# Kernel tuning notes

Measured on AMD Instinct MI355X. Metric: run time of the kernel, lower is better.

Reference implementation:

```python
import jax, jax.numpy as jnp
import numpy as np

B = 65536      # batch
IN = 784       # 1*28*28 flattened input
H = 768        # hidden_size
D = 3          # num_domains
E = 64         # expert hidden
C = 10         # classes
EPS = 1e-5     # BatchNorm eps


def setup_inputs() -> dict:
    key = jax.random.key(0)
    ks = jax.random.split(key, 8)
    s = lambda k, shp, sc: (jax.random.normal(k, shp, jnp.float32) * sc)
    return dict(
        x=jax.random.normal(ks[0], (B, 1, 28, 28), jnp.float32),
        # pre_classifier: Linear(784, H) + BatchNorm1d(H) affine params
        W1=s(ks[1], (IN, H), 0.03), b1=jnp.zeros((H,), jnp.float32),
        gamma=jnp.ones((H,), jnp.float32), beta=jnp.zeros((H,), jnp.float32),
        # discriminator: Linear(H,H) -> ReLU -> Linear(H,D)
        Wd1=s(ks[2], (H, H), 0.03), bd1=jnp.zeros((H,), jnp.float32),
        Wd2=s(ks[3], (H, D), 0.03), bd2=jnp.zeros((D,), jnp.float32),
        # per-domain expert classifiers: Linear(H,64) -> ReLU -> Linear(64,10), stacked over D
        Wa=s(ks[4], (D, H, E), 0.03), ba=jnp.zeros((D, E), jnp.float32),
        Wb=s(ks[5], (D, E, C), 0.1), bb=jnp.zeros((D, C), jnp.float32),
    )


def reference(x, W1, b1, gamma, beta, Wd1, bd1, Wd2, bd2, Wa, ba, Wb, bb):
    xf = x.reshape(x.shape[0], -1)                      # [B, 784]
    h = xf @ W1 + b1                                    # [B, H]
    # BatchNorm1d in training mode: batch mean / biased variance
    mu = h.mean(axis=0)
    var = jnp.mean((h - mu) ** 2, axis=0)
    feat = jax.nn.relu((h - mu) / jnp.sqrt(var + EPS) * gamma + beta)  # [B, H]
    # ReverseLayerF with alpha=0: identity forward, zero gradient back to feat
    rev = jax.lax.stop_gradient(feat)
    dom_out = jax.nn.relu(rev @ Wd1 + bd1) @ Wd2 + bd2  # [B, D]
    dom_pred = jnp.argmax(dom_out, axis=1)              # [B] int routing
    # hard routing: compute all D tiny experts densely, select by dom_pred
    hid = jax.nn.relu(jnp.einsum('bh,dhe->bde', feat, Wa) + ba)   # [B, D, E]
    all_out = jnp.einsum('bde,dec->bdc', hid, Wb) + bb            # [B, D, C]
    outs = jnp.take_along_axis(all_out, dom_pred[:, None, None], axis=1)[:, 0, :]  # [B, C]
    return outs, dom_out
```

## Files before the change

### kernel.cpp

```cpp
#include <hip/hip_runtime.h>
#include <math.h>

#define BATCH 65536
#define KIN   784
#define HD    768

typedef float f32x4 __attribute__((ext_vector_type(4)));
typedef short s16x8 __attribute__((ext_vector_type(8)));
typedef unsigned int __attribute__((address_space(3))) lds_u32;
typedef const unsigned int __attribute__((address_space(1))) glb_u32;

__device__ __forceinline__ float frelu(float x){ return x > 0.f ? x : 0.f; }

__device__ __forceinline__ unsigned int cvtpk(float a, float b){
    unsigned int r;
    asm("v_cvt_pk_bf16_f32 %0, %1, %2" : "=v"(r) : "v"(a), "v"(b));
    return r;
}
__device__ __forceinline__ unsigned short f2bf(float v){
    unsigned int u = __builtin_bit_cast(unsigned int, v);
    u += 0x7FFFu + ((u >> 16) & 1u);
    return (unsigned short)(u >> 16);
}
__device__ __forceinline__ float bf2f(unsigned short s){
    unsigned int u = ((unsigned int)s) << 16;
    return __builtin_bit_cast(float, u);
}
__device__ __forceinline__ void gload16(const void* g, void* l){
    __builtin_amdgcn_global_load_lds((glb_u32*)g, (lds_u32*)l, 16, 0, 0);
}

__global__ __launch_bounds__(256)
void cvtX(const float* __restrict__ x, unsigned short* __restrict__ xbf)
{
    int idx = blockIdx.x * 256 + threadIdx.x;
    int row = idx / 104, c = (idx - row * 104) * 8;
    uint4 o = make_uint4(0, 0, 0, 0);
    if (c < KIN) {
        const float* p = x + (size_t)row * KIN + c;
        float4 a = *(const float4*)p;
        float4 b = *(const float4*)(p + 4);
        o.x = cvtpk(a.x, a.y); o.y = cvtpk(a.z, a.w);
        o.z = cvtpk(b.x, b.y); o.w = cvtpk(b.z, b.w);
    }
    *(uint4*)(xbf + (size_t)row * 832 + c) = o;
}

__global__ __launch_bounds__(256)
void featBN(const unsigned short* __restrict__ hbf,
            const float* __restrict__ scale, const float* __restrict__ shift,
            unsigned short* __restrict__ fbf)
{
    int idx = blockIdx.x * 256 + threadIdx.x;
    int row = idx / 96, c = (idx - row * 96) * 8;
    s16x8 hv = *(const s16x8*)(hbf + (size_t)row * HD + c);
    float4 s0 = *(const float4*)(scale + c), s1 = *(const float4*)(scale + c + 4);
    float4 t0 = *(const float4*)(shift + c), t1 = *(const float4*)(shift + c + 4);
    float v[8];
    v[0] = frelu(bf2f((unsigned short)hv[0]) * s0.x + t0.x);
    v[1] = frelu(bf2f((unsigned short)hv[1]) * s0.y + t0.y);
    v[2] = frelu(bf2f((unsigned short)hv[2]) * s0.z + t0.z);
    v[3] = frelu(bf2f((unsigned short)hv[3]) * s0.w + t0.w);
    v[4] = frelu(bf2f((unsigned short)hv[4]) * s1.x + t1.x);
    v[5] = frelu(bf2f((unsigned short)hv[5]) * s1.y + t1.y);
    v[6] = frelu(bf2f((unsigned short)hv[6]) * s1.z + t1.z);
    v[7] = frelu(bf2f((unsigned short)hv[7]) * s1.w + t1.w);
    uint4 o;
    o.x = cvtpk(v[0], v[1]); o.y = cvtpk(v[2], v[3]);
    o.z = cvtpk(v[4], v[5]); o.w = cvtpk(v[6], v[7]);
    *(uint4*)(fbf + (size_t)row * HD + c) = o;
}

__global__ __launch_bounds__(256)
void tileW(const float* __restrict__ W, char* __restrict__ Wh, int K, int N, int NT)
{
    int chunk = blockIdx.x;
    int nb = chunk / NT, t = chunk - nb * NT;
    int tid = threadIdx.x;
    #pragma unroll
    for (int q = 0; q < 2; q++) {
        int idx = q * 256 + tid;
        int r = idx >> 2, p = idx & 3;
        int s = (p ^ ((r >> 1) & 3)) & 3;
        int kb = t * 32 + s * 8;
        int n = nb * 128 + r;
        s16x8 hv;
        #pragma unroll
        for (int e = 0; e < 8; e++) {
            int k = kb + e;
            float v = (k < K) ? W[(size_t)k * N + n] : 0.f;
            hv[e] = (short)f2bf(v);
        }
        *(s16x8*)(Wh + (size_t)chunk * 8192 + idx * 16) = hv;
    }
}

__global__ __launch_bounds__(256)
void tileWa(const float* __restrict__ Wa, char* __restrict__ WaC)
{
    int chunk = blockIdx.x;
    int d = chunk / 24, t = chunk - d * 24;
    int idx = threadIdx.x;
    int r = idx >> 2, p = idx & 3;
    int s = (p ^ ((r >> 1) & 3)) & 3;
    int kb = t * 32 + s * 8;
    s16x8 hv;
    #pragma unroll
    for (int e = 0; e < 8; e++)
        hv[e] = (short)f2bf(Wa[((size_t)d * HD + kb + e) * 64 + r]);
    *(s16x8*)(WaC + (size_t)chunk * 4096 + idx * 16) = hv;
}

template<int MODE>
__global__ __launch_bounds__(256, 3)
void gemm97(const unsigned short* __restrict__ Abf,
            const char* __restrict__ BhC,
            const float* __restrict__ bias,
            unsigned short* __restrict__ Hbf,
            const float* __restrict__ Wd2, double* __restrict__ domacc,
            float* __restrict__ sp1, float* __restrict__ sp2,
            int KP, int NT)
{
    __shared__ __align__(16) char sm[32768];

    int bid = blockIdx.x;
    int wg = (bid & 7) * 384 + (bid >> 3);
    int mb = wg / 6, nb = wg - mb * 6;
    int m0 = mb << 7, n0 = nb << 7;

    int tid = threadIdx.x;
    int lane = tid & 63, wid = tid >> 6;
    int wr = wid >> 1, wc = wid & 1;
    int l15 = lane & 15, l4 = lane >> 4;

    int aoff[4], boff[4];
    #pragma unroll
    for (int f = 0; f < 4; f++) {
        int ra = wr * 64 + f * 16 + l15;
        aoff[f] = ra * 64 + (((l4 ^ (ra >> 1)) & 3) << 4);
        int rb = wc * 64 + f * 16 + l15;
        boff[f] = rb * 64 + (((l4 ^ (rb >> 1)) & 3) << 4);
    }

    int ar[2], asl[2];
    #pragma unroll
    for (int q = 0; q < 2; q++) {
        int idx = q * 256 + tid;
        int r = idx >> 2, p = idx & 3;
        asl[q] = (p ^ ((r >> 1) & 3)) & 3;
        ar[q] = r;
    }

    f32x4 acc[4][4];
    #pragma unroll
    for (int i = 0; i < 4; i++)
        #pragma unroll
        for (int j = 0; j < 4; j++) acc[i][j] = (f32x4){0.f, 0.f, 0.f, 0.f};

    int NTc = 2 * NT;
    for (int t = 0; t < NT; t++) {
        int t2 = 2 * t;
        #pragma unroll
        for (int h = 0; h < 2; h++) {
            #pragma unroll
            for (int q = 0; q < 2; q++) {
                const unsigned short* src = Abf + (size_t)(m0 + ar[q]) * KP
                                          + (t2 + h) * 32 + asl[q] * 8;
                gload16(src, sm + h * 8192 + (q * 256 + tid) * 16);
            }
        }
        #pragma unroll
        for (int h = 0; h < 2; h++) {
            size_t cb = (size_t)(nb * NTc + t2 + h) * 8192;
            #pragma unroll
            for (int q = 0; q < 2; q++) {
                int off = (q * 256 + tid) * 16;
                gload16(BhC + cb + off, sm + 16384 + h * 8192 + off);
            }
        }
        __syncthreads();
        #pragma unroll
        for (int h = 0; h < 2; h++) {
            const char* ab  = sm + h * 8192;
            const char* bb2 = sm + 16384 + h * 8192;
            s16x8 fah[4], fbh[4];
            #pragma unroll
            for (int f = 0; f < 4; f++) {
                fah[f] = *(const s16x8*)(ab + aoff[f]);
                fbh[f] = *(const s16x8*)(bb2 + boff[f]);
            }
            #pragma unroll
            for (int i = 0; i < 4; i++)
                #pragma unroll
                for (int j = 0; j < 4; j++)
                    acc[i][j] = __builtin_amdgcn_mfma_f32_16x16x32_bf16(fah[i], fbh[j], acc[i][j], 0, 0, 0);
        }
        __syncthreads();
    }

    if (MODE == 0) {
        float bc[4];
        #pragma unroll
        for (int f = 0; f < 4; f++) bc[f] = bias[n0 + wc * 64 + f * 16 + l15];
        float cs[4] = {0.f,0.f,0.f,0.f}, cq[4] = {0.f,0.f,0.f,0.f};
        #pragma unroll
        for (int i = 0; i < 4; i++) {
            int rowb = m0 + wr * 64 + i * 16 + l4 * 4;
            #pragma unroll
            for (int j2 = 0; j2 < 4; j2++) {
                unsigned short* hrow = Hbf + (size_t)(rowb + j2) * HD + n0 + wc * 64 + l15;
                #pragma unroll
                for (int f = 0; f < 4; f++) {
                    float v = acc[i][f][j2] + bc[f];
                    hrow[f * 16] = (unsigned short)cvtpk(v, v);
                    cs[f] += v; cq[f] += v * v;
                }
            }
        }
        #pragma unroll
        for (int m = 16; m < 64; m <<= 1)
            #pragma unroll
            for (int f = 0; f < 4; f++) {
                cs[f] += __shfl_xor(cs[f], m, 64);
                cq[f] += __shfl_xor(cq[f], m, 64);
            }
        if (l4 == 0) {
            #pragma unroll
            for (int f = 0; f < 4; f++) {
                int col = n0 + wc * 64 + f * 16 + l15;
                sp1[(size_t)col * 1024 + mb * 2 + wr] = cs[f];
                sp2[(size_t)col * 1024 + mb * 2 + wr] = cq[f];
            }
        }
    } else {
        float bc[4], w2[4][3];
        #pragma unroll
        for (int f = 0; f < 4; f++) {
            int col = n0 + wc * 64 + f * 16 + l15;
            bc[f] = bias[col];
            w2[f][0] = Wd2[col * 3 + 0]; w2[f][1] = Wd2[col * 3 + 1]; w2[f][2] = Wd2[col * 3 + 2];
        }
        float s0[16], s1[16], s2[16];
        #pragma unroll
        for (int i = 0; i < 16; i++) { s0[i] = 0.f; s1[i] = 0.f; s2[i] = 0.f; }
        #pragma unroll
        for (int i = 0; i < 4; i++)
            #pragma unroll
            for (int j2 = 0; j2 < 4; j2++) {
                int idx = i * 4 + j2;
                #pragma unroll
                for (int f = 0; f < 4; f++) {
                    float v = frelu(acc[i][f][j2] + bc[f]);
                    s0[idx] += v * w2[f][0];
                    s1[idx] += v * w2[f][1];
                    s2[idx] += v * w2[f][2];
                }
            }
        #pragma unroll
        for (int m = 1; m < 16; m <<= 1) {
            #pragma unroll
            for (int i = 0; i < 16; i++) {
                s0[i] += __shfl_xor(s0[i], m, 64);
                s1[i] += __shfl_xor(s1[i], m, 64);
                s2[i] += __shfl_xor(s2[i], m, 64);
            }
        }
        if (l15 == 0) {
            #pragma unroll
            for (int i = 0; i < 16; i++) {
                int row = m0 + wr * 64 + (i >> 2) * 16 + l4 * 4 + (i & 3);
                atomicAdd(&domacc[(size_t)row * 3 + 0], (double)s0[i]);
                atomicAdd(&domacc[(size_t)row * 3 + 1], (double)s1[i]);
                atomicAdd(&domacc[(size_t)row * 3 + 2], (double)s2[i]);
            }
        }
    }
}

__global__ __launch_bounds__(256)
void bnfinal(const float* __restrict__ sp1, const float* __restrict__ sp2,
             const float* __restrict__ gamma, const float* __restrict__ beta,
             float* __restrict__ scale, float* __restrict__ shift)
{
    int c = blockIdx.x, t = threadIdx.x;
    const float* p1 = sp1 + (size_t)c * 1024;
    const float* p2 = sp2 + (size_t)c * 1024;
    double S = (double)p1[t] + (double)p1[t + 256] + (double)p1[t + 512] + (double)p1[t + 768];
    double Q = (double)p2[t] + (double)p2[t + 256] + (double)p2[t + 512] + (double)p2[t + 768];
    #pragma unroll
    for (int m = 1; m < 64; m <<= 1) { S += __shfl_xor(S, m, 64); Q += __shfl_xor(Q, m, 64); }
    __shared__ double sd1[4], sd2[4];
    int w = t >> 6;
    if ((t & 63) == 0) { sd1[w] = S; sd2[w] = Q; }
    __syncthreads();
    if (t == 0) {
        double Sa = sd1[0] + sd1[1] + sd1[2] + sd1[3];
        double Qa = sd2[0] + sd2[1] + sd2[2] + sd2[3];
        double mu  = Sa * (1.0 / 65536.0);
        double var = Qa * (1.0 / 65536.0) - mu * mu;
        double inv = 1.0 / sqrt(var + 1e-5);
        double sc  = inv * (double)gamma[c];
        double sh  = (double)beta[c] - mu * sc;
        scale[c] = (float)sc;
        shift[c] = (float)sh;
    }
}

__global__ __launch_bounds__(256)
void domfinal_a(const double* __restrict__ domacc, const float* __restrict__ bd2,
                float* __restrict__ outdom, int* __restrict__ fixmeta, int* __restrict__ fixlist)
{
    int r = blockIdx.x * 256 + threadIdx.x;
    double v0 = domacc[(size_t)r * 3 + 0] + (double)bd2[0];
    double v1 = domacc[(size_t)r * 3 + 1] + (double)bd2[1];
    double v2 = domacc[(size_t)r * 3 + 2] + (double)bd2[2];
    outdom[(size_t)r * 3 + 0] = (float)v0;
    outdom[(size_t)r * 3 + 1] = (float)v1;
    outdom[(size_t)r * 3 + 2] = (float)v2;
    double mx01 = v0 > v1 ? v0 : v1, mn01 = v0 > v1 ? v1 : v0;
    double best = mx01 > v2 ? mx01 : v2;
    double m2   = mx01 > v2 ? (mn01 > v2 ? mn01 : v2) : mx01;
    if (best - m2 < 1.5e-2) {
        int p = atomicAdd(fixmeta, 1);
        fixlist[p] = r;
    }
}

#define FR 8
__global__ __launch_bounds__(256)
void fixrow_x(const int* __restrict__ fixmeta, const int* __restrict__ fixlist,
              const float* __restrict__ x, const float* __restrict__ W1,
              const float* __restrict__ b1,
              const float* __restrict__ scale, const float* __restrict__ shift,
              const float* __restrict__ Wd1, const float* __restrict__ bd1,
              const float* __restrict__ Wd2, const float* __restrict__ bd2,
              float* __restrict__ outdom)
{
    int nfix = fixmeta[0];
    __shared__ float xs[FR][788];
    __shared__ float ft[FR][HD];
    __shared__ float red[4][3];
    int tid = threadIdx.x;
    int n0 = tid * 3;
    for (int base = blockIdx.x * FR; base < nfix; base += gridDim.x * FR) {
        int nr = nfix - base; if (nr > FR) nr = FR;
        __syncthreads();
        for (int i = tid; i < FR * KIN; i += 256) {
            int rr = i / KIN, c = i - rr * KIN;
            int row = fixlist[base + (rr < nr ? rr : nr - 1)];
            xs[rr][c] = x[(size_t)row * KIN + c];
        }
        __syncthreads();
        {
            float acc[FR][3];
            #pragma unroll
            for (int r = 0; r < FR; r++) { acc[r][0]=0.f; acc[r][1]=0.f; acc[r][2]=0.f; }
            for (int k = 0; k < KIN; k++) {
                float w0 = W1[(size_t)k * HD + n0];
                float w1 = W1[(size_t)k * HD + n0 + 1];
                float w2 = W1[(size_t)k * HD + n0 + 2];
                #pragma unroll
                for (int r = 0; r < FR; r++) {
                    float xv = xs[r][k];
                    acc[r][0] += xv * w0; acc[r][1] += xv * w1; acc[r][2] += xv * w2;
                }
            }
            #pragma unroll
            for (int j = 0; j < 3; j++) {
                float bj = b1[n0 + j], scj = scale[n0 + j], shj = shift[n0 + j];
                #pragma unroll
                for (int r = 0; r < FR; r++)
                    ft[r][n0 + j] = frelu((acc[r][j] + bj) * scj + shj);
            }
        }
        __syncthreads();
        float acc[FR][3];
        #pragma unroll
        for (int r = 0; r < FR; r++) { acc[r][0]=0.f; acc[r][1]=0.f; acc[r][2]=0.f; }
        for (int k = 0; k < HD; k++) {
            float w0 = Wd1[(size_t)k * HD + n0];
            float w1 = Wd1[(size_t)k * HD + n0 + 1];
            float w2 = Wd1[(size_t)k * HD + n0 + 2];
            #pragma unroll
            for (int r = 0; r < FR; r++) {
                float fv = ft[r][k];
                acc[r][0] += fv * w0; acc[r][1] += fv * w1; acc[r][2] += fv * w2;
            }
        }
        float b0 = bd1[n0], b1v = bd1[n0 + 1], b2 = bd1[n0 + 2];
        float wa[3][3];
        #pragma unroll
        for (int i = 0; i < 3; i++)
            #pragma unroll
            for (int d = 0; d < 3; d++) wa[i][d] = Wd2[(n0 + i) * 3 + d];
        #pragma unroll
        for (int r = 0; r < FR; r++) {
            if (r >= nr) break;
            float h0 = frelu(acc[r][0] + b0);
            float h1 = frelu(acc[r][1] + b1v);
            float h2 = frelu(acc[r][2] + b2);
            float y0 = h0 * wa[0][0] + h1 * wa[1][0] + h2 * wa[2][0];
            float y1 = h0 * wa[0][1] + h1 * wa[1][1] + h2 * wa[2][1];
            float y2 = h0 * wa[0][2] + h1 * wa[1][2] + h2 * wa[2][2];
            #pragma unroll
            for (int m = 1; m < 64; m <<= 1) {
                y0 += __shfl_xor(y0, m, 64);
                y1 += __shfl_xor(y1, m, 64);
                y2 += __shfl_xor(y2, m, 64);
            }
            if ((tid & 63) == 0) { red[tid >> 6][0] = y0; red[tid >> 6][1] = y1; red[tid >> 6][2] = y2; }
            __syncthreads();
            if (tid == 0) {
                int row = fixlist[base + r];
                double v0 = (double)red[0][0] + red[1][0] + red[2][0] + red[3][0] + (double)bd2[0];
                double v1 = (double)red[0][1] + red[1][1] + red[2][1] + red[3][1] + (double)bd2[1];
                double v2 = (double)red[0][2] + red[1][2] + red[2][2] + red[3][2] + (double)bd2[2];
                outdom[(size_t)row * 3 + 0] = (float)v0;
                outdom[(size_t)row * 3 + 1] = (float)v1;
                outdom[(size_t)row * 3 + 2] = (float)v2;
            }
            __syncthreads();
        }
    }
}

__global__ __launch_bounds__(256)
void domfinal_b(const float* __restrict__ outdom, int* __restrict__ cnt, int* __restrict__ lists)
{
    __shared__ int lcnt[3], base[3];
    int tid = threadIdx.x;
    if (tid < 3) lcnt[tid] = 0;
    __syncthreads();
    int r = blockIdx.x * 256 + tid;
    float v0 = outdom[(size_t)r * 3 + 0];
    float v1 = outdom[(size_t)r * 3 + 1];
    float v2 = outdom[(size_t)r * 3 + 2];
    int p = 0; float best = v0;
    if (v1 > best) { best = v1; p = 1; }
    if (v2 > best) { best = v2; p = 2; }
    int lpos = atomicAdd(&lcnt[p], 1);
    __syncthreads();
    if (tid < 3) base[tid] = atomicAdd(&cnt[tid], lcnt[tid]);
    __syncthreads();
    lists[(size_t)p * BATCH + base[p] + lpos] = r;
}

__global__ __launch_bounds__(256)
void expert_mfma(const unsigned short* __restrict__ fbf,
                 const char* __restrict__ WaC,
                 const int* __restrict__ cnt, const int* __restrict__ lists,
                 const float* __restrict__ ba,
                 const float* __restrict__ Wb, const float* __restrict__ bb,
                 float* __restrict__ outs)
{
    __shared__ __align__(16) char sm[12288];
    __shared__ float hid[128][66];
    __shared__ int rowidx[128];

    int d = blockIdx.y;
    int count = cnt[d];
    int start = blockIdx.x * 128;
    if (start >= count) return;
    int nrows = count - start; if (nrows > 128) nrows = 128;

    int tid = threadIdx.x;
    int lane = tid & 63, wid = tid >> 6;
    int l15 = lane & 15, l4 = lane >> 4;

    if (tid < 128) {
        int i = tid < nrows ? tid : nrows - 1;
        rowidx[tid] = lists[(size_t)d * BATCH + start + i];
    }
    __syncthreads();

    int asl[2], arow[2];
    #pragma unroll
    for (int q = 0; q < 2; q++) {
        int idx = q * 256 + tid;
        int r = idx >> 2, p = idx & 3;
        asl[q] = (p ^ ((r >> 1) & 3)) & 3;
        arow[q] = rowidx[r];
    }

    int aoff[2], boff[4];
    #pragma unroll
    for (int i2 = 0; i2 < 2; i2++) {
        int ra = wid * 32 + i2 * 16 + l15;
        aoff[i2] = ra * 64 + (((l4 ^ (ra >> 1)) & 3) << 4);
    }
    #pragma unroll
    for (int f = 0; f < 4; f++) {
        int rb = f * 16 + l15;
        boff[f] = rb * 64 + (((l4 ^ (rb >> 1)) & 3) << 4);
    }

    f32x4 acc[2][4];
    #pragma unroll
    for (int i = 0; i < 2; i++)
        #pragma unroll
        for (int j = 0; j < 4; j++) acc[i][j] = (f32x4){0.f, 0.f, 0.f, 0.f};

    for (int t = 0; t < 24; t++) {
        #pragma unroll
        for (int q = 0; q < 2; q++)
            gload16(fbf + (size_t)arow[q] * HD + t * 32 + asl[q] * 8,
                    sm + (q * 256 + tid) * 16);
        gload16(WaC + (size_t)(d * 24 + t) * 4096 + tid * 16, sm + 8192 + tid * 16);
        __syncthreads();
        s16x8 fa[2], fb[4];
        #pragma unroll
        for (int i2 = 0; i2 < 2; i2++) fa[i2] = *(const s16x8*)(sm + aoff[i2]);
        #pragma unroll
        for (int f = 0; f < 4; f++)    fb[f]  = *(const s16x8*)(sm + 8192 + boff[f]);
        #pragma unroll
        for (int i2 = 0; i2 < 2; i2++)
            #pragma unroll
            for (int f = 0; f < 4; f++)
                acc[i2][f] = __builtin_amdgcn_mfma_f32_16x16x32_bf16(fa[i2], fb[f], acc[i2][f], 0, 0, 0);
        __syncthreads();
    }

    #pragma unroll
    for (int i2 = 0; i2 < 2; i2++)
        #pragma unroll
        for (int f = 0; f < 4; f++) {
            int col = f * 16 + l15;
            float bav = ba[d * 64 + col];
            #pragma unroll
            for (int j = 0; j < 4; j++) {
                int row = wid * 32 + i2 * 16 + l4 * 4 + j;
                hid[row][col] = frelu(acc[i2][f][j] + bav);
            }
        }
    __syncthreads();

    for (int o = tid; o < 1280; o += 256) {
        int r2 = o / 10, c = o - r2 * 10;
        if (r2 < nrows) {
            float s = 0.f;
            #pragma unroll 16
            for (int l = 0; l < 64; l++) s += hid[r2][l] * Wb[((size_t)d * 64 + l) * 10 + c];
            outs[(size_t)rowidx[r2] * 10 + c] = s + bb[d * 10 + c];
        }
    }
}

extern "C" void kernel_launch(void* const* d_in, const int* in_sizes, int n_in,
                              void* d_out, int out_size, void* d_ws, size_t ws_size,
                              hipStream_t stream)
{
    const float* x     = (const float*)d_in[0];
    const float* W1    = (const float*)d_in[1];
    const float* b1    = (const float*)d_in[2];
    const float* gamma = (const float*)d_in[3];
    const float* beta  = (const float*)d_in[4];
    const float* Wd1   = (const float*)d_in[5];
    const float* bd1   = (const float*)d_in[6];
    const float* Wd2   = (const float*)d_in[7];
    const float* bd2   = (const float*)d_in[8];
    const float* Wa    = (const float*)d_in[9];
    const float* ba    = (const float*)d_in[10];
    const float* Wb    = (const float*)d_in[11];
    const float* bb    = (const float*)d_in[12];

    float* out    = (float*)d_out;
    float* outs   = out;
    float* outdom = out + (size_t)BATCH * 10;

    const int NT1 = 13, NT2 = 12;
    const int NTC1 = 26, NTC2 = 24;

    char* ws = (char*)d_ws;
    size_t off = 0;
    unsigned short* hbf = (unsigned short*)(ws + off); off += (size_t)BATCH * HD * 2;
    unsigned short* xbf = (unsigned short*)(ws + off); off += (size_t)BATCH * 832 * 2;
    unsigned short* fbf = xbf;
    char*  W1hC   = ws + off;            off += (size_t)6 * NTC1 * 8192;
    char*  Wd1hC  = ws + off;            off += (size_t)6 * NTC2 * 8192;
    char*  WaC    = ws + off;            off += (size_t)3 * 24 * 4096;
    float* sp1    = (float*)(ws + off);  off += (size_t)HD * 1024 * 4;
    float* sp2    = (float*)(ws + off);  off += (size_t)HD * 1024 * 4;
    float* scale  = (float*)(ws + off);  off += HD * 4;
    float* shift  = (float*)(ws + off);  off += HD * 4;
    size_t zoff = off;
    double* domacc = (double*)(ws + off); off += (size_t)BATCH * 3 * 8;
    int*    cnt    = (int*)(ws + off);    off += 64;
    int*    fixmeta= (int*)(ws + off);    off += 64;
    size_t zbytes = off - zoff;
    int*    lists  = (int*)(ws + off);    off += (size_t)3 * BATCH * 4;
    int*    fixlist= (int*)(ws + off);    off += (size_t)BATCH * 4;

    hipMemsetAsync(ws + zoff, 0, zbytes, stream);

    tileW<<<6 * NTC1, 256, 0, stream>>>(W1, W1hC, KIN, HD, NTC1);
    tileW<<<6 * NTC2, 256, 0, stream>>>(Wd1, Wd1hC, HD, HD, NTC2);
    tileWa<<<72, 256, 0, stream>>>(Wa, WaC);
    cvtX<<<BATCH * 104 / 256, 256, 0, stream>>>(x, xbf);

    gemm97<0><<<3072, 256, 0, stream>>>(xbf, W1hC, b1, hbf,
                                        nullptr, nullptr, sp1, sp2, 832, NT1);
    bnfinal<<<HD, 256, 0, stream>>>(sp1, sp2, gamma, beta, scale, shift);
    featBN<<<BATCH * 96 / 256, 256, 0, stream>>>(hbf, scale, shift, fbf);
    gemm97<1><<<3072, 256, 0, stream>>>(fbf, Wd1hC, bd1, nullptr,
                                        Wd2, domacc, nullptr, nullptr, HD, NT2);
    domfinal_a<<<BATCH / 256, 256, 0, stream>>>(domacc, bd2, outdom, fixmeta, fixlist);
    fixrow_x<<<256, 256, 0, stream>>>(fixmeta, fixlist, x, W1, b1, scale, shift,
                                      Wd1, bd1, Wd2, bd2, outdom);
    domfinal_b<<<BATCH / 256, 256, 0, stream>>>(outdom, cnt, lists);
    dim3 eg(512, 3);
    expert_mfma<<<eg, 256, 0, stream>>>(fbf, WaC, cnt, lists, ba, Wb, bb, outs);
}
```

Before: 695.5 us.

## Recompute near-tie routing rows with split-bf16 MFMA GEMMs instead of scalar loops

Replaces the scalar FP32 fix-up kernel for rows with ambiguous domain argmax with two MFMA GEMM kernels. These use a three-product hi/lo bf16 split (hi*hi + hi*lo + lo*hi) to approximate FP32 accuracy, plus a finalize kernel. The weights are pre-split into hi and lo tiled copies. The goal is to cut the cost of the slow per-row scalar recomputation. It adds extra tiling writes and workspace, and caps the number of fix rows at a fixed capacity, which could drop rows if too many are near-ties.

```diff
diff --git a/kernel.cpp b/kernel.cpp
--- a/kernel.cpp
+++ b/kernel.cpp
@@ -4,6 +4,7 @@
 #define BATCH 65536
 #define KIN   784
 #define HD    768
+#define FCAP  16384
 
 typedef float f32x4 __attribute__((ext_vector_type(4)));
 typedef short s16x8 __attribute__((ext_vector_type(8)));
@@ -72,7 +73,8 @@
 }
 
 __global__ __launch_bounds__(256)
-void tileW(const float* __restrict__ W, char* __restrict__ Wh, int K, int N, int NT)
+void tileW(const float* __restrict__ W, char* __restrict__ Wh, char* __restrict__ Wl,
+           int K, int N, int NT)
 {
     int chunk = blockIdx.x;
     int nb = chunk / NT, t = chunk - nb * NT;
@@ -84,14 +86,17 @@
         int s = (p ^ ((r >> 1) & 3)) & 3;
         int kb = t * 32 + s * 8;
         int n = nb * 128 + r;
-        s16x8 hv;
+        s16x8 hv, lv;
         #pragma unroll
         for (int e = 0; e < 8; e++) {
             int k = kb + e;
             float v = (k < K) ? W[(size_t)k * N + n] : 0.f;
-            hv[e] = (short)f2bf(v);
+            unsigned short h = f2bf(v);
+            hv[e] = (short)h;
+            lv[e] = (short)f2bf(v - bf2f(h));
         }
         *(s16x8*)(Wh + (size_t)chunk * 8192 + idx * 16) = hv;
+        *(s16x8*)(Wl + (size_t)chunk * 8192 + idx * 16) = lv;
     }
 }
 
@@ -326,101 +331,289 @@
     }
 }
 
-#define FR 8
-__global__ __launch_bounds__(256)
-void fixrow_x(const int* __restrict__ fixmeta, const int* __restrict__ fixlist,
-              const float* __restrict__ x, const float* __restrict__ W1,
-              const float* __restrict__ b1,
-              const float* __restrict__ scale, const float* __restrict__ shift,
-              const float* __restrict__ Wd1, const float* __restrict__ bd1,
-              const float* __restrict__ Wd2, const float* __restrict__ bd2,
-              float* __restrict__ outdom)
-{
-    int nfix = fixmeta[0];
-    __shared__ float xs[FR][788];
-    __shared__ float ft[FR][HD];
-    __shared__ float red[4][3];
+__global__ __launch_bounds__(256)
+void gfix1(const int* __restrict__ fixmeta, const int* __restrict__ fixlist,
+           const float* __restrict__ x,
+           const char* __restrict__ BhC, const char* __restrict__ BlC,
+           const float* __restrict__ b1, const float* __restrict__ scale,
+           const float* __restrict__ shift,
+           unsigned short* __restrict__ ffh, unsigned short* __restrict__ ffl)
+{
+    __shared__ __align__(16) char sm[32768];
+    __shared__ int rowidx[128];
+    int nfix = fixmeta[0]; if (nfix > FCAP) nfix = FCAP;
+    int start = blockIdx.x * 128;
+    if (start >= nfix) return;
+    int nb = blockIdx.y;
+    int n0 = nb << 7;
+
     int tid = threadIdx.x;
-    int n0 = tid * 3;
-    for (int base = blockIdx.x * FR; base < nfix; base += gridDim.x * FR) {
-        int nr = nfix - base; if (nr > FR) nr = FR;
+    int lane = tid & 63, wid = tid >> 6;
+    int wr = wid >> 1, wc = wid & 1;
+    int l15 = lane & 15, l4 = lane >> 4;
+
+    if (tid < 128) {
+        int i = start + tid;
+        rowidx[tid] = fixlist[i < nfix ? i : nfix - 1];
+    }
+    __syncthreads();
+
+    int aoff[4], boff[4];
+    #pragma unroll
+    for (int f = 0; f < 4; f++) {
+        int ra = wr * 64 + f * 16 + l15;
+        aoff[f] = ra * 64 + (((l4 ^ (ra >> 1)) & 3) << 4);
+        int rb = wc * 64 + f * 16 + l15;
+        boff[f] = rb * 64 + (((l4 ^ (rb >> 1)) & 3) << 4);
+    }
+    int ar[2], asl[2], arow[2];
+    #pragma unroll
+    for (int q = 0; q < 2; q++) {
+        int idx = q * 256 + tid;
+        int r = idx >> 2, p = idx & 3;
+        asl[q] = (p ^ ((r >> 1) & 3)) & 3;
+        ar[q] = r;
+        arow[q] = rowidx[r];
+    }
+
+    f32x4 acc[4][4];
+    #pragma unroll
+    for (int i = 0; i < 4; i++)
+        #pragma unroll
+        for (int j = 0; j < 4; j++) acc[i][j] = (f32x4){0.f, 0.f, 0.f, 0.f};
+
+    float av[2][8];
+    auto loadA = [&](int t) {
+        #pragma unroll
+        for (int q = 0; q < 2; q++) {
+            int kb = t * 32 + asl[q] * 8;
+            const float* src = x + (size_t)arow[q] * KIN + kb;
+            if (kb + 7 < KIN) {
+                *(float4*)&av[q][0] = *(const float4*)src;
+                *(float4*)&av[q][4] = *(const float4*)(src + 4);
+            } else {
+                #pragma unroll
+                for (int e = 0; e < 8; e++) av[q][e] = (kb + e < KIN) ? src[e] : 0.f;
+            }
+        }
+    };
+    auto writeA = [&]() {
+        #pragma unroll
+        for (int q = 0; q < 2; q++) {
+            int idx = q * 256 + tid;
+            float* v = av[q];
+            uint4 oh;
+            oh.x = cvtpk(v[0], v[1]); oh.y = cvtpk(v[2], v[3]);
+            oh.z = cvtpk(v[4], v[5]); oh.w = cvtpk(v[6], v[7]);
+            float h0 = bf2f((unsigned short)(oh.x & 0xFFFF));
+            float h1 = bf2f((unsigned short)(oh.x >> 16));
+            float h2 = bf2f((unsigned short)(oh.y & 0xFFFF));
+            float h3 = bf2f((unsigned short)(oh.y >> 16));
+            float h4 = bf2f((unsigned short)(oh.z & 0xFFFF));
+            float h5 = bf2f((unsigned short)(oh.z >> 16));
+            float h6 = bf2f((unsigned short)(oh.w & 0xFFFF));
+            float h7 = bf2f((unsigned short)(oh.w >> 16));
+            uint4 ol;
+            ol.x = cvtpk(v[0] - h0, v[1] - h1); ol.y = cvtpk(v[2] - h2, v[3] - h3);
+            ol.z = cvtpk(v[4] - h4, v[5] - h5); ol.w = cvtpk(v[6] - h6, v[7] - h7);
+            *(uint4*)(sm + idx * 16) = oh;
+            *(uint4*)(sm + 8192 + idx * 16) = ol;
+        }
+    };
+
+    loadA(0);
+    const int NTc = 26;
+    for (int t = 0; t < NTc; t++) {
         __syncthreads();
-        for (int i = tid; i < FR * KIN; i += 256) {
-            int rr = i / KIN, c = i - rr * KIN;
-            int row = fixlist[base + (rr < nr ? rr : nr - 1)];
-            xs[rr][c] = x[(size_t)row * KIN + c];
-        }
+        size_t cb = (size_t)(nb * NTc + t) * 8192;
+        #pragma unroll
+        for (int q = 0; q < 2; q++) {
+            int off = (q * 256 + tid) * 16;
+            gload16(BhC + cb + off, sm + 16384 + off);
+            gload16(BlC + cb + off, sm + 24576 + off);
+        }
+        writeA();
+        if (t + 1 < NTc) loadA(t + 1);
         __syncthreads();
-        {
-            float acc[FR][3];
-            #pragma unroll
-            for (int r = 0; r < FR; r++) { acc[r][0]=0.f; acc[r][1]=0.f; acc[r][2]=0.f; }
-            for (int k = 0; k < KIN; k++) {
-                float w0 = W1[(size_t)k * HD + n0];
-                float w1 = W1[(size_t)k * HD + n0 + 1];
-                float w2 = W1[(size_t)k * HD + n0 + 2];
+        s16x8 fah[4], fal[4], fbh[4], fbl[4];
+        #pragma unroll
+        for (int f = 0; f < 4; f++) {
+            fah[f] = *(const s16x8*)(sm + aoff[f]);
+            fal[f] = *(const s16x8*)(sm + 8192 + aoff[f]);
+            fbh[f] = *(const s16x8*)(sm + 16384 + boff[f]);
+            fbl[f] = *(const s16x8*)(sm + 24576 + boff[f]);
+        }
+        #pragma unroll
+        for (int i = 0; i < 4; i++)
+            #pragma unroll
+            for (int j = 0; j < 4; j++) {
+                acc[i][j] = __builtin_amdgcn_mfma_f32_16x16x32_bf16(fah[i], fbl[j], acc[i][j], 0, 0, 0);
+                acc[i][j] = __builtin_amdgcn_mfma_f32_16x16x32_bf16(fal[i], fbh[j], acc[i][j], 0, 0, 0);
+                acc[i][j] = __builtin_amdgcn_mfma_f32_16x16x32_bf16(fah[i], fbh[j], acc[i][j], 0, 0, 0);
+            }
+    }
+
+    float bc[4], sc[4], sh[4];
+    #pragma unroll
+    for (int f = 0; f < 4; f++) {
+        int col = n0 + wc * 64 + f * 16 + l15;
+        bc[f] = b1[col]; sc[f] = scale[col]; sh[f] = shift[col];
+    }
+    #pragma unroll
+    for (int i = 0; i < 4; i++) {
+        #pragma unroll
+        for (int j2 = 0; j2 < 4; j2++) {
+            int pos = start + wr * 64 + i * 16 + l4 * 4 + j2;
+            if (pos < nfix) {
                 #pragma unroll
-                for (int r = 0; r < FR; r++) {
-                    float xv = xs[r][k];
-                    acc[r][0] += xv * w0; acc[r][1] += xv * w1; acc[r][2] += xv * w2;
+                for (int f = 0; f < 4; f++) {
+                    int col = n0 + wc * 64 + f * 16 + l15;
+                    float fl = frelu((acc[i][f][j2] + bc[f]) * sc[f] + sh[f]);
+                    unsigned short hi = (unsigned short)cvtpk(fl, fl);
+                    unsigned short lo = (unsigned short)cvtpk(fl - bf2f(hi), 0.f);
+                    ffh[(size_t)pos * HD + col] = hi;
+                    ffl[(size_t)pos * HD + col] = lo;
                 }
             }
-            #pragma unroll
-            for (int j = 0; j < 3; j++) {
-                float bj = b1[n0 + j], scj = scale[n0 + j], shj = shift[n0 + j];
-                #pragma unroll
-                for (int r = 0; r < FR; r++)
-                    ft[r][n0 + j] = frelu((acc[r][j] + bj) * scj + shj);
-            }
+        }
+    }
+}
+
+__global__ __launch_bounds__(256)
+void gfix2(const int* __restrict__ fixmeta,
+           const unsigned short* __restrict__ ffh, const unsigned short* __restrict__ ffl,
+           const char* __restrict__ BhC, const char* __restrict__ BlC,
+           const float* __restrict__ bd1, const float* __restrict__ Wd2,
+           double* __restrict__ domfix)
+{
+    __shared__ __align__(16) char sm[32768];
+    int nfix = fixmeta[0]; if (nfix > FCAP) nfix = FCAP;
+    int start = blockIdx.x * 128;
+    if (start >= nfix) return;
+    int nb = blockIdx.y;
+    int n0 = nb << 7;
+
+    int tid = threadIdx.x;
+    int lane = tid & 63, wid = tid >> 6;
+    int wr = wid >> 1, wc = wid & 1;
+    int l15 = lane & 15, l4 = lane >> 4;
+
+    int aoff[4], boff[4];
+    #pragma unroll
+    for (int f = 0; f < 4; f++) {
+        int ra = wr * 64 + f * 16 + l15;
+        aoff[f] = ra * 64 + (((l4 ^ (ra >> 1)) & 3) << 4);
+        int rb = wc * 64 + f * 16 + l15;
+        boff[f] = rb * 64 + (((l4 ^ (rb >> 1)) & 3) << 4);
+    }
+    int arow[2], asl[2];
+    #pragma unroll
+    for (int q = 0; q < 2; q++) {
+        int idx = q * 256 + tid;
+        int r = idx >> 2, p = idx & 3;
+        asl[q] = (p ^ ((r >> 1) & 3)) & 3;
+        int pos = start + r;
+        arow[q] = pos < nfix ? pos : nfix - 1;
+    }
+
+    f32x4 acc[4][4];
+    #pragma unroll
+    for (int i = 0; i < 4; i++)
+        #pragma unroll
+        for (int j = 0; j < 4; j++) acc[i][j] = (f32x4){0.f, 0.f, 0.f, 0.f};
+
+    const int NTc = 24;
+    for (int t = 0; t < NTc; t++) {
+        #pragma unroll
+        for (int q = 0; q < 2; q++) {
+            size_t ao = (size_t)arow[q] * HD + t * 32 + asl[q] * 8;
+            gload16(ffh + ao, sm + (q * 256 + tid) * 16);
+            gload16(ffl + ao, sm + 8192 + (q * 256 + tid) * 16);
+        }
+        size_t cb = (size_t)(nb * NTc + t) * 8192;
+        #pragma unroll
+        for (int q = 0; q < 2; q++) {
+            int off = (q * 256 + tid) * 16;
+            gload16(BhC + cb + off, sm + 16384 + off);
+            gload16(BlC + cb + off, sm + 24576 + off);
         }
         __syncthreads();
-        float acc[FR][3];
-        #pragma unroll
-        for (int r = 0; r < FR; r++) { acc[r][0]=0.f; acc[r][1]=0.f; acc[r][2]=0.f; }
-        for (int k = 0; k < HD; k++) {
-            float w0 = Wd1[(size_t)k * HD + n0];
-            float w1 = Wd1[(size_t)k * HD + n0 + 1];
-            float w2 = Wd1[(size_t)k * HD + n0 + 2];
-            #pragma unroll
-            for (int r = 0; r < FR; r++) {
-                float fv = ft[r][k];
-                acc[r][0] += fv * w0; acc[r][1] += fv * w1; acc[r][2] += fv * w2;
-            }
-        }
-        float b0 = bd1[n0], b1v = bd1[n0 + 1], b2 = bd1[n0 + 2];
-        float wa[3][3];
-        #pragma unroll
-        for (int i = 0; i < 3; i++)
-            #pragma unroll
-            for (int d = 0; d < 3; d++) wa[i][d] = Wd2[(n0 + i) * 3 + d];
-        #pragma unroll
-        for (int r = 0; r < FR; r++) {
-            if (r >= nr) break;
-            float h0 = frelu(acc[r][0] + b0);
-            float h1 = frelu(acc[r][1] + b1v);
-            float h2 = frelu(acc[r][2] + b2);
-            float y0 = h0 * wa[0][0] + h1 * wa[1][0] + h2 * wa[2][0];
-            float y1 = h0 * wa[0][1] + h1 * wa[1][1] + h2 * wa[2][1];
-            float y2 = h0 * wa[0][2] + h1 * wa[1][2] + h2 * wa[2][2];
-            #pragma unroll
-            for (int m = 1; m < 64; m <<= 1) {
-                y0 += __shfl_xor(y0, m, 64);
-                y1 += __shfl_xor(y1, m, 64);
-                y2 += __shfl_xor(y2, m, 64);
-            }
-            if ((tid & 63) == 0) { red[tid >> 6][0] = y0; red[tid >> 6][1] = y1; red[tid >> 6][2] = y2; }
-            __syncthreads();
-            if (tid == 0) {
-                int row = fixlist[base + r];
-                double v0 = (double)red[0][0] + red[1][0] + red[2][0] + red[3][0] + (double)bd2[0];
-                double v1 = (double)red[0][1] + red[1][1] + red[2][1] + red[3][1] + (double)bd2[1];
-                double v2 = (double)red[0][2] + red[1][2] + red[2][2] + red[3][2] + (double)bd2[2];
-                outdom[(size_t)row * 3 + 0] = (float)v0;
-                outdom[(size_t)row * 3 + 1] = (float)v1;
-                outdom[(size_t)row * 3 + 2] = (float)v2;
-            }
-            __syncthreads();
-        }
+        s16x8 fah[4], fal[4], fbh[4], fbl[4];
+        #pragma unroll
+        for (int f = 0; f < 4; f++) {
+            fah[f] = *(const s16x8*)(sm + aoff[f]);
+            fal[f] = *(const s16x8*)(sm + 8192 + aoff[f]);
+            fbh[f] = *(const s16x8*)(sm + 16384 + boff[f]);
+            fbl[f] = *(const s16x8*)(sm + 24576 + boff[f]);
+        }
+        #pragma unroll
+        for (int i = 0; i < 4; i++)
+            #pragma unroll
+            for (int j = 0; j < 4; j++) {
+                acc[i][j] = __builtin_amdgcn_mfma_f32_16x16x32_bf16(fah[i], fbl[j], acc[i][j], 0, 0, 0);
+                acc[i][j] = __builtin_amdgcn_mfma_f32_16x16x32_bf16(fal[i], fbh[j], acc[i][j], 0, 0, 0);
+                acc[i][j] = __builtin_amdgcn_mfma_f32_16x16x32_bf16(fah[i], fbh[j], acc[i][j], 0, 0, 0);
+            }
+        __syncthreads();
+    }
+
+    float bc[4], w2[4][3];
+    #pragma unroll
+    for (int f = 0; f < 4; f++) {
+        int col = n0 + wc * 64 + f * 16 + l15;
+        bc[f] = bd1[col];
+        w2[f][0] = Wd2[col * 3 + 0]; w2[f][1] = Wd2[col * 3 + 1]; w2[f][2] = Wd2[col * 3 + 2];
+    }
+    float s0[16], s1[16], s2[16];
+    #pragma unroll
+    for (int i = 0; i < 16; i++) { s0[i] = 0.f; s1[i] = 0.f; s2[i] = 0.f; }
+    #pragma unroll
+    for (int i = 0; i < 4; i++)
+        #pragma unroll
+        for (int j2 = 0; j2 < 4; j2++) {
+            int idx = i * 4 + j2;
+            #pragma unroll
+            for (int f = 0; f < 4; f++) {
+                float v = frelu(acc[i][f][j2] + bc[f]);
+                s0[idx] += v * w2[f][0];
+                s1[idx] += v * w2[f][1];
+                s2[idx] += v * w2[f][2];
+            }
+        }
+    #pragma unroll
+    for (int m = 1; m < 16; m <<= 1) {
+        #pragma unroll
+        for (int i = 0; i < 16; i++) {
+            s0[i] += __shfl_xor(s0[i], m, 64);
+            s1[i] += __shfl_xor(s1[i], m, 64);
+            s2[i] += __shfl_xor(s2[i], m, 64);
+        }
+    }
+    if (l15 == 0) {
+        #pragma unroll
+        for (int i = 0; i < 16; i++) {
+            int pos = start + wr * 64 + (i >> 2) * 16 + l4 * 4 + (i & 3);
+            if (pos < nfix) {
+                atomicAdd(&domfix[(size_t)pos * 3 + 0], (double)s0[i]);
+                atomicAdd(&domfix[(size_t)pos * 3 + 1], (double)s1[i]);
+                atomicAdd(&domfix[(size_t)pos * 3 + 2], (double)s2[i]);
+            }
+        }
+    }
+}
+
+__global__ __launch_bounds__(256)
+void fixfin(const int* __restrict__ fixmeta, const int* __restrict__ fixlist,
+            const double* __restrict__ domfix, const float* __restrict__ bd2,
+            float* __restrict__ outdom)
+{
+    int nfix = fixmeta[0]; if (nfix > FCAP) nfix = FCAP;
+    int i = blockIdx.x * 256 + threadIdx.x;
+    if (i < nfix) {
+        int row = fixlist[i];
+        outdom[(size_t)row * 3 + 0] = (float)(domfix[(size_t)i * 3 + 0] + (double)bd2[0]);
+        outdom[(size_t)row * 3 + 1] = (float)(domfix[(size_t)i * 3 + 1] + (double)bd2[1]);
+        outdom[(size_t)row * 3 + 2] = (float)(domfix[(size_t)i * 3 + 2] + (double)bd2[2]);
     }
 }
 
@@ -575,8 +768,12 @@
     unsigned short* hbf = (unsigned short*)(ws + off); off += (size_t)BATCH * HD * 2;
     unsigned short* xbf = (unsigned short*)(ws + off); off += (size_t)BATCH * 832 * 2;
     unsigned short* fbf = xbf;
+    unsigned short* ffh = hbf;
+    unsigned short* ffl = hbf + (size_t)FCAP * HD;
     char*  W1hC   = ws + off;            off += (size_t)6 * NTC1 * 8192;
+    char*  W1loC  = ws + off;            off += (size_t)6 * NTC1 * 8192;
     char*  Wd1hC  = ws + off;            off += (size_t)6 * NTC2 * 8192;
+    char*  Wd1loC = ws + off;            off += (size_t)6 * NTC2 * 8192;
     char*  WaC    = ws + off;            off += (size_t)3 * 24 * 4096;
     float* sp1    = (float*)(ws + off);  off += (size_t)HD * 1024 * 4;
     float* sp2    = (float*)(ws + off);  off += (size_t)HD * 1024 * 4;
@@ -584,6 +781,7 @@
     float* shift  = (float*)(ws + off);  off += HD * 4;
     size_t zoff = off;
     double* domacc = (double*)(ws + off); off += (size_t)BATCH * 3 * 8;
+    double* domfix = (double*)(ws + off); off += (size_t)FCAP * 3 * 8;
     int*    cnt    = (int*)(ws + off);    off += 64;
     int*    fixmeta= (int*)(ws + off);    off += 64;
     size_t zbytes = off - zoff;
@@ -592,8 +790,8 @@
 
     hipMemsetAsync(ws + zoff, 0, zbytes, stream);
 
-    tileW<<<6 * NTC1, 256, 0, stream>>>(W1, W1hC, KIN, HD, NTC1);
-    tileW<<<6 * NTC2, 256, 0, stream>>>(Wd1, Wd1hC, HD, HD, NTC2);
+    tileW<<<6 * NTC1, 256, 0, stream>>>(W1, W1hC, W1loC, KIN, HD, NTC1);
+    tileW<<<6 * NTC2, 256, 0, stream>>>(Wd1, Wd1hC, Wd1loC, HD, HD, NTC2);
     tileWa<<<72, 256, 0, stream>>>(Wa, WaC);
     cvtX<<<BATCH * 104 / 256, 256, 0, stream>>>(x, xbf);
 
@@ -604,8 +802,14 @@
     gemm97<1><<<3072, 256, 0, stream>>>(fbf, Wd1hC, bd1, nullptr,
                                         Wd2, domacc, nullptr, nullptr, HD, NT2);
     domfinal_a<<<BATCH / 256, 256, 0, stream>>>(domacc, bd2, outdom, fixmeta, fixlist);
-    fixrow_x<<<256, 256, 0, stream>>>(fixmeta, fixlist, x, W1, b1, scale, shift,
-                                      Wd1, bd1, Wd2, bd2, outdom);
+    {
+        dim3 fg(FCAP / 128, 6);
+        gfix1<<<fg, 256, 0, stream>>>(fixmeta, fixlist, x, W1hC, W1loC,
+                                      b1, scale, shift, ffh, ffl);
+        gfix2<<<fg, 256, 0, stream>>>(fixmeta, ffh, ffl, Wd1hC, Wd1loC,
+                                      bd1, Wd2, domfix);
+        fixfin<<<FCAP / 256, 256, 0, stream>>>(fixmeta, fixlist, domfix, bd2, outdom);
+    }
     domfinal_b<<<BATCH / 256, 256, 0, stream>>>(outdom, cnt, lists);
     dim3 eg(512, 3);
     expert_mfma<<<eg, 256, 0, stream>>>(fbf, WaC, cnt, lists, ba, Wb, bb, outs);
```

New measurement: 573.2 us, median of 3. 1.21x faster.
